# Kernel tuning notes

Hardware: AMD Instinct MI355X
Metric: run time of the kernel (lower is better)

The kernel has to match this reference:

```python
import jax, jax.numpy as jnp
import numpy as np

EPS = 1e-6

def _rms_norm(x, w):
    rms = jnp.sqrt(jnp.mean(x * x, axis=-1, keepdims=True) + EPS)
    return x / rms * w

def _rotate_half(x):
    x1, x2 = jnp.split(x, 2, axis=-1)
    return jnp.concatenate([-x2, x1], axis=-1)

def _apply_rope(qk, cos, sin):
    return qk * cos + _rotate_half(qk) * sin

def setup_inputs() -> dict:
    key = jax.random.key(0)
    ks = jax.random.split(key, 4)
    B, N, C, H = 4, 2048, 1024, 16
    hd = C // H
    x = jax.random.normal(ks[0], (B, N, C), dtype=jnp.float32)
    rope_cos = jax.random.uniform(ks[1], (1, 1, N, hd), dtype=jnp.float32)
    rope_sin = jax.random.uniform(ks[2], (1, 1, N, hd), dtype=jnp.float32)
    w_qkv = jax.random.normal(ks[3], (3 * C, C), dtype=jnp.float32) * (C ** -0.5)
    w_proj = jax.random.normal(jax.random.fold_in(key, 10), (C, C), dtype=jnp.float32) * (C ** -0.5)
    b_proj = jnp.zeros((C,), dtype=jnp.float32)
    q_norm_w = jnp.ones((hd,), dtype=jnp.float32)
    k_norm_w = jnp.ones((hd,), dtype=jnp.float32)
    return {"x": x, "rope_cos": rope_cos, "rope_sin": rope_sin, "w_qkv": w_qkv,
            "w_proj": w_proj, "b_proj": b_proj, "q_norm_w": q_norm_w, "k_norm_w": k_norm_w}

def reference(x, rope_cos, rope_sin, w_qkv, w_proj, b_proj, q_norm_w, k_norm_w):
    B, N, C = x.shape
    H = 16
    hd = C // H
    scale = hd ** -0.5
    qkv = jnp.einsum('bnc,dc->bnd', x, w_qkv)          # [B,N,3C]
    qkv = qkv.reshape(B, N, 3, H, hd).transpose(2, 0, 3, 1, 4)  # [3,B,H,N,hd]
    q, k, v = qkv[0], qkv[1], qkv[2]
    q = _rms_norm(q, q_norm_w)
    k = _rms_norm(k, k_norm_w)
    q = _apply_rope(q, rope_cos, rope_sin)
    k = _apply_rope(k, rope_cos, rope_sin)
    attn = jnp.einsum('bhqd,bhkd->bhqk', q, k) * scale
    attn = jax.nn.softmax(attn, axis=-1)
    out = jnp.einsum('bhqk,bhkd->bhqd', attn, v)        # [B,H,N,hd]
    out = out.transpose(0, 2, 1, 3).reshape(B, N, C)
    return jnp.einsum('bnc,dc->bnd', out, w_proj) + b_proj
```

## Files before the change

kernel.cpp:

```cpp
#include <hip/hip_runtime.h>
#include <stdint.h>
#include <math.h>

typedef unsigned short u16;
typedef __attribute__((ext_vector_type(8))) short short8;
typedef __attribute__((ext_vector_type(4))) float floatx4;
typedef __attribute__((ext_vector_type(4))) unsigned short ushort4v;

#define MFMA16(a, b, c) __builtin_amdgcn_mfma_f32_16x16x32_bf16(a, b, c, 0, 0, 0)

constexpr int B_ = 4, N_ = 2048, C_ = 1024, H_ = 16, HD = 64;
constexpr size_t SZ_X = (size_t)B_ * N_ * C_;
constexpr size_t SZ_WQKV = (size_t)3 * C_ * C_;
constexpr size_t SZ_WPROJ = (size_t)C_ * C_;
constexpr size_t SZ_QKV = (size_t)B_ * H_ * N_ * HD;

#define QSCALE 0.1803368801111204f

__device__ __forceinline__ u16 f2bf(float f) {
  union { float f; uint32_t u; } c; c.f = f;
  uint32_t u = c.u;
  return (u16)((u + 0x7FFFu + ((u >> 16) & 1u)) >> 16);
}
__device__ __forceinline__ uint32_t p2b(float s) {
  return (uint32_t)(int)__builtin_fmaf(s, 128.0f, 16250.91f);
}
__device__ __forceinline__ void async16(const u16* g, u16* l) {
  __builtin_amdgcn_global_load_lds(
      (const __attribute__((address_space(1))) void*)g,
      (__attribute__((address_space(3))) void*)l, 16, 0, 0);
}

__global__ __launch_bounds__(256) void cvt_bf16(const float* __restrict__ in,
                                                u16* __restrict__ out, int n4) {
  int i = blockIdx.x * 256 + threadIdx.x;
  if (i >= n4) return;
  float4 v = ((const float4*)in)[i];
  ushort4v o;
  o.x = f2bf(v.x); o.y = f2bf(v.y); o.z = f2bf(v.z); o.w = f2bf(v.w);
  ((ushort4v*)out)[i] = o;
}

template <int MODE>
__global__ __launch_bounds__(256) void gemm_bt(
    const u16* __restrict__ A, const u16* __restrict__ Bm, int K,
    u16* __restrict__ qb, u16* __restrict__ kb, u16* __restrict__ vtb,
    float* __restrict__ outf, const float* __restrict__ bias, int N,
    const float* __restrict__ cosp, const float* __restrict__ sinp,
    const float* __restrict__ qw, const float* __restrict__ kw) {
  const int tid = threadIdx.x;
  const int wave = tid >> 6;
  const int lane = tid & 63;
  const int quad = lane >> 4;
  const int l16 = lane & 15;
  const int id = blockIdx.x + blockIdx.y * 64;
  const int bm0 = ((id & 7) * 8 + ((id >> 3) & 7)) * 128;
  const int bn0 = (id >> 6) * 128;
  const int wm = (wave >> 1) * 64;
  const int wn = (wave & 1) * 64;

  __shared__ __align__(16) u16 As[2][128 * 32];
  __shared__ __align__(16) u16 Bs[2][128 * 32];

  floatx4 acc[4][4];
#pragma unroll
  for (int i = 0; i < 4; ++i)
#pragma unroll
    for (int j = 0; j < 4; ++j)
#pragma unroll
      for (int r = 0; r < 4; ++r) acc[i][j][r] = 0.f;

  auto stage = [&](int k0, int buf) {
#pragma unroll
    for (int j = 0; j < 2; ++j) {
      const int seg = tid + j * 256;
      const int row = seg >> 2;
      const int ks = (seg & 3) * 8;
      u16* la = As[buf] + (size_t)(wave * 64 + j * 256) * 8;
      u16* lb = Bs[buf] + (size_t)(wave * 64 + j * 256) * 8;
      async16(A + (size_t)(bm0 + row) * K + k0 + ks, la);
      async16(Bm + (size_t)(bn0 + row) * K + k0 + ks, lb);
    }
  };

  const int niter = K >> 5;
  stage(0, 0);
  for (int kt = 0; kt < niter; ++kt) {
    __syncthreads();
    if (kt + 1 < niter) stage((kt + 1) << 5, (kt + 1) & 1);
    const u16* as = As[kt & 1];
    const u16* bs = Bs[kt & 1];

    short8 af[4], bf[4];
#pragma unroll
    for (int t = 0; t < 4; ++t)
      af[t] = *(const short8*)(as + (wm + t * 16 + l16) * 32 + quad * 8);
#pragma unroll
    for (int t = 0; t < 4; ++t)
      bf[t] = *(const short8*)(bs + (wn + t * 16 + l16) * 32 + quad * 8);
#pragma unroll
    for (int i = 0; i < 4; ++i)
#pragma unroll
      for (int j = 0; j < 4; ++j)
        acc[i][j] = MFMA16(af[i], bf[j], acc[i][j]);
  }

  if (MODE == 0) {
    const int hb = (bn0 + wn) >> 6;
    const int t = hb >> 4;
    const int h = hb & 15;
    if (t < 2) {
      const float* w = (t == 0) ? qw : kw;
      u16* dstb = (t == 0) ? qb : kb;
      float wv[4];
#pragma unroll
      for (int j = 0; j < 4; ++j) wv[j] = w[j * 16 + l16];
#pragma unroll
      for (int i = 0; i < 4; ++i)
#pragma unroll
        for (int r = 0; r < 4; ++r) {
          const int m = bm0 + wm + i * 16 + quad * 4 + r;
          const int b = m >> 11, tok = m & 2047;
          float ss = 0.f;
#pragma unroll
          for (int j = 0; j < 4; ++j) ss += acc[i][j][r] * acc[i][j][r];
          ss += __shfl_xor(ss, 1);
          ss += __shfl_xor(ss, 2);
          ss += __shfl_xor(ss, 4);
          ss += __shfl_xor(ss, 8);
          const float inv = 1.0f / sqrtf(ss * (1.0f / 64.0f) + 1e-6f);
          float xn[4];
#pragma unroll
          for (int j = 0; j < 4; ++j) xn[j] = acc[i][j][r] * inv * wv[j];
          u16* dst = dstb + ((size_t)(b * 16 + h) * 2048 + tok) * 64;
#pragma unroll
          for (int j = 0; j < 4; ++j) {
            const int e = j * 16 + l16;
            const float cs = cosp[tok * 64 + e];
            const float sn = sinp[tok * 64 + e];
            const float rot = (j < 2) ? -xn[j + 2] : xn[j - 2];
            float o = xn[j] * cs + rot * sn;
            if (t == 0) o *= QSCALE;
            dst[e] = f2bf(o);
          }
        }
    } else {
#pragma unroll
      for (int i = 0; i < 4; ++i)
#pragma unroll
        for (int j = 0; j < 4; ++j)
#pragma unroll
          for (int r = 0; r < 4; ++r) {
            const int m = bm0 + wm + i * 16 + quad * 4 + r;
            const int b = m >> 11, tok = m & 2047;
            const int e = j * 16 + l16;
            vtb[((size_t)(b * 16 + h) * 64 + e) * 2048 + tok] =
                f2bf(acc[i][j][r]);
          }
    }
  } else {
#pragma unroll
    for (int i = 0; i < 4; ++i)
#pragma unroll
      for (int j = 0; j < 4; ++j)
#pragma unroll
        for (int r = 0; r < 4; ++r) {
          const int m = bm0 + wm + i * 16 + quad * 4 + r;
          const int n = bn0 + wn + j * 16 + l16;
          outf[(size_t)m * N + n] = acc[i][j][r] + bias[n];
        }
  }
}

__global__ __launch_bounds__(256) void attn_kernel(
    const u16* __restrict__ qb, const u16* __restrict__ kb,
    const u16* __restrict__ vtb, u16* __restrict__ ob) {
  const int tid = threadIdx.x;
  const int wave = tid >> 6, lane = tid & 63;
  const int quad = lane >> 4, l16 = lane & 15;

  const int id = blockIdx.x + blockIdx.y * 16;
  const int bh = (id & 7) + 8 * ((id >> 3) & 7);
  const int q0 = (id >> 6) * 128;

  __shared__ __align__(16) u16 Ksf[2][64 * 64];
  __shared__ __align__(16) u16 Vsf[2][64 * 64];
  __shared__ __align__(16) u16 Ps[4][2][16 * 72];

  const u16* qptr = qb + (size_t)bh * (2048 * 64);
  const u16* kptr = kb + (size_t)bh * (2048 * 64);
  const u16* vptr = vtb + (size_t)bh * (64 * 2048);

  const int s0 = tid, s1 = tid + 256;
  const int ct0 = s0 >> 7, ct1 = s1 >> 7;
  const int hf0 = (s0 >> 6) & 1, hf1 = (s1 >> 6) & 1;
  const u16* kg0 = kptr + (size_t)(ct0 * 16 + l16) * 64 + hf0 * 32 + quad * 8;
  const u16* kg1 = kptr + (size_t)(ct1 * 16 + l16) * 64 + hf1 * 32 + quad * 8;
  const u16* vg0 = vptr + (size_t)(ct0 * 16 + l16) * 2048 + hf0 * 32 + quad * 8;
  const u16* vg1 = vptr + (size_t)(ct1 * 16 + l16) * 2048 + hf1 * 32 + quad * 8;
  const int lo0 = (wave * 64) * 8;
  const int lo1 = (256 + wave * 64) * 8;

  short8 aq[2][2];
#pragma unroll
  for (int sub = 0; sub < 2; ++sub) {
    const int qrow = q0 + wave * 32 + sub * 16 + l16;
#pragma unroll
    for (int hf = 0; hf < 2; ++hf)
      aq[sub][hf] =
          *(const short8*)(qptr + (size_t)qrow * 64 + hf * 32 + quad * 8);
  }

  short8 ones;
#pragma unroll
  for (int j = 0; j < 8; ++j) ones[j] = (short)0x3F80;

  floatx4 o[2][4], ol[2];
#pragma unroll
  for (int sub = 0; sub < 2; ++sub) {
#pragma unroll
    for (int r = 0; r < 4; ++r) ol[sub][r] = 0.f;
#pragma unroll
    for (int et = 0; et < 4; ++et)
#pragma unroll
      for (int r = 0; r < 4; ++r) o[sub][et][r] = 0.f;
  }

  async16(kg0, Ksf[0] + lo0);
  async16(kg1, Ksf[0] + lo1);
  async16(vg0, Vsf[0] + lo0);
  async16(vg1, Vsf[0] + lo1);

  for (int it = 0; it < 32; ++it) {
    __syncthreads();
    if (it + 1 < 32) {
      const int n1 = (it + 1) * 64;
      const int b1 = (it + 1) & 1;
      async16(kg0 + (size_t)n1 * 64, Ksf[b1] + lo0);
      async16(kg1 + (size_t)n1 * 64, Ksf[b1] + lo1);
      async16(vg0 + n1, Vsf[b1] + lo0);
      async16(vg1 + n1, Vsf[b1] + lo1);
    }
    const u16* Kt = Ksf[it & 1];
    const u16* Vt = Vsf[it & 1];

#pragma unroll
    for (int t = 0; t < 4; ++t) {
      const short8 kf0 = *(const short8*)(Kt + t * 1024 + lane * 8);
      const short8 kf1 = *(const short8*)(Kt + t * 1024 + 512 + lane * 8);
#pragma unroll
      for (int sub = 0; sub < 2; ++sub) {
        floatx4 z;
#pragma unroll
        for (int r = 0; r < 4; ++r) z[r] = 0.f;
        z = MFMA16(kf0, aq[sub][0], z);
        z = MFMA16(kf1, aq[sub][1], z);
        uint2 w;
        w.x = p2b(z[0]) | (p2b(z[1]) << 16);
        w.y = p2b(z[2]) | (p2b(z[3]) << 16);
        *(uint2*)(Ps[wave][sub] + l16 * 72 + t * 16 + quad * 4) = w;
      }
    }

    __asm__ volatile("s_waitcnt lgkmcnt(0)" ::: "memory");

    short8 pa[2][2];
#pragma unroll
    for (int sub = 0; sub < 2; ++sub) {
      pa[sub][0] = *(const short8*)(Ps[wave][sub] + l16 * 72 + quad * 8);
      pa[sub][1] = *(const short8*)(Ps[wave][sub] + l16 * 72 + 32 + quad * 8);
    }

#pragma unroll
    for (int et = 0; et < 4; ++et) {
      const short8 vb0 = *(const short8*)(Vt + et * 1024 + lane * 8);
      const short8 vb1 = *(const short8*)(Vt + et * 1024 + 512 + lane * 8);
#pragma unroll
      for (int sub = 0; sub < 2; ++sub) {
        o[sub][et] = MFMA16(pa[sub][0], vb0, o[sub][et]);
        o[sub][et] = MFMA16(pa[sub][1], vb1, o[sub][et]);
      }
    }
#pragma unroll
    for (int sub = 0; sub < 2; ++sub) {
      ol[sub] = MFMA16(pa[sub][0], ones, ol[sub]);
      ol[sub] = MFMA16(pa[sub][1], ones, ol[sub]);
    }
  }

  const int b = bh >> 4, h = bh & 15;
#pragma unroll
  for (int sub = 0; sub < 2; ++sub) {
    float inv[4];
#pragma unroll
    for (int r = 0; r < 4; ++r) inv[r] = 1.0f / ol[sub][r];
#pragma unroll
    for (int et = 0; et < 4; ++et)
#pragma unroll
      for (int r = 0; r < 4; ++r) {
        const int row = q0 + wave * 32 + sub * 16 + quad * 4 + r;
        const int e = et * 16 + l16;
        ob[((size_t)b * 2048 + row) * 1024 + h * 64 + e] =
            f2bf(o[sub][et][r] * inv[r]);
      }
  }
}

extern "C" void kernel_launch(void* const* d_in, const int* in_sizes, int n_in,
                              void* d_out, int out_size, void* d_ws, size_t ws_size,
                              hipStream_t stream) {
  const float* x     = (const float*)d_in[0];
  const float* cosp  = (const float*)d_in[1];
  const float* sinp  = (const float*)d_in[2];
  const float* wqkv  = (const float*)d_in[3];
  const float* wproj = (const float*)d_in[4];
  const float* bias  = (const float*)d_in[5];
  const float* qw    = (const float*)d_in[6];
  const float* kw    = (const float*)d_in[7];
  float* out = (float*)d_out;

  u16* xb     = (u16*)d_ws;
  u16* wqkvb  = xb + SZ_X;
  u16* wprojb = wqkvb + SZ_WQKV;
  u16* qb     = wprojb + SZ_WPROJ;
  u16* kb     = qb + SZ_QKV;
  u16* vtb    = kb + SZ_QKV;
  u16* ob     = vtb + SZ_QKV;

  cvt_bf16<<<(int)(SZ_X / 4 / 256), 256, 0, stream>>>(x, xb, (int)(SZ_X / 4));
  cvt_bf16<<<(int)(SZ_WQKV / 4 / 256), 256, 0, stream>>>(wqkv, wqkvb, (int)(SZ_WQKV / 4));
  cvt_bf16<<<(int)(SZ_WPROJ / 4 / 256), 256, 0, stream>>>(wproj, wprojb, (int)(SZ_WPROJ / 4));

  gemm_bt<0><<<dim3(64, 24), 256, 0, stream>>>(xb, wqkvb, 1024, qb, kb, vtb,
                                               nullptr, nullptr, 3072,
                                               cosp, sinp, qw, kw);
  attn_kernel<<<dim3(16, 64), 256, 0, stream>>>(qb, kb, vtb, ob);
  gemm_bt<1><<<dim3(64, 8), 256, 0, stream>>>(ob, wprojb, 1024, nullptr, nullptr,
                                              nullptr, out, bias, 1024,
                                              nullptr, nullptr, nullptr, nullptr);
}
```

Baseline: 305.0 us.

## Pre-swizzle K/V into MFMA fragment layout and load V directly from global

The QKV GEMM epilogue now writes K and V^T in a tile-blocked layout that matches the MFMA fragment order, so the attention kernel copies K contiguously into LDS and reads V fragments straight from global memory into registers without staging through shared memory. This removes the V LDS buffer and halves the async copies per iteration, and launch bounds now request 4 blocks per CU for higher occupancy. The three conversion kernels are also merged into one launch to cut launch overhead. In exchange, the epilogue stores become more scattered, and V global loads sit on the critical path without LDS double-buffering, relying on occupancy to hide their latency.

```diff
diff --git a/kernel.cpp b/kernel.cpp
--- a/kernel.cpp
+++ b/kernel.cpp
@@ -31,14 +31,22 @@
       (__attribute__((address_space(3))) void*)l, 16, 0, 0);
 }
 
-__global__ __launch_bounds__(256) void cvt_bf16(const float* __restrict__ in,
-                                                u16* __restrict__ out, int n4) {
+__global__ __launch_bounds__(256) void cvt_all(
+    const float* __restrict__ x, const float* __restrict__ wqkv,
+    const float* __restrict__ wproj, u16* __restrict__ xb,
+    u16* __restrict__ wqkvb, u16* __restrict__ wprojb) {
+  const int n1 = (int)(SZ_X / 4), n2 = (int)(SZ_WQKV / 4);
   int i = blockIdx.x * 256 + threadIdx.x;
-  if (i >= n4) return;
-  float4 v = ((const float4*)in)[i];
+  const float* src;
+  u16* dst;
+  int k;
+  if (i < n1) { src = x; dst = xb; k = i; }
+  else if (i < n1 + n2) { src = wqkv; dst = wqkvb; k = i - n1; }
+  else { src = wproj; dst = wprojb; k = i - n1 - n2; }
+  float4 v = ((const float4*)src)[k];
   ushort4v o;
   o.x = f2bf(v.x); o.y = f2bf(v.y); o.z = f2bf(v.z); o.w = f2bf(v.w);
-  ((ushort4v*)out)[i] = o;
+  ((ushort4v*)dst)[k] = o;
 }
 
 template <int MODE>
@@ -111,7 +119,6 @@
     const int h = hb & 15;
     if (t < 2) {
       const float* w = (t == 0) ? qw : kw;
-      u16* dstb = (t == 0) ? qb : kb;
       float wv[4];
 #pragma unroll
       for (int j = 0; j < 4; ++j) wv[j] = w[j * 16 + l16];
@@ -132,7 +139,7 @@
           float xn[4];
 #pragma unroll
           for (int j = 0; j < 4; ++j) xn[j] = acc[i][j][r] * inv * wv[j];
-          u16* dst = dstb + ((size_t)(b * 16 + h) * 2048 + tok) * 64;
+          const size_t bh = (size_t)(b * 16 + h);
 #pragma unroll
           for (int j = 0; j < 4; ++j) {
             const int e = j * 16 + l16;
@@ -140,8 +147,15 @@
             const float sn = sinp[tok * 64 + e];
             const float rot = (j < 2) ? -xn[j + 2] : xn[j - 2];
             float o = xn[j] * cs + rot * sn;
-            if (t == 0) o *= QSCALE;
-            dst[e] = f2bf(o);
+            if (t == 0) {
+              qb[(bh * 2048 + tok) * 64 + e] = f2bf(o * QSCALE);
+            } else {
+              const int kt2 = tok >> 6, t3 = (tok >> 4) & 3;
+              const int hf = j >> 1;
+              const int qf = (j & 1) * 2 + (l16 >> 3);
+              kb[bh * 131072 + (size_t)kt2 * 4096 + (t3 * 2 + hf) * 512 +
+                 (qf * 16 + (tok & 15)) * 8 + (l16 & 7)] = f2bf(o);
+            }
           }
         }
     } else {
@@ -153,8 +167,10 @@
           for (int r = 0; r < 4; ++r) {
             const int m = bm0 + wm + i * 16 + quad * 4 + r;
             const int b = m >> 11, tok = m & 2047;
-            const int e = j * 16 + l16;
-            vtb[((size_t)(b * 16 + h) * 64 + e) * 2048 + tok] =
+            const int kt2 = tok >> 6, nn = tok & 63;
+            const int hf = nn >> 5, qf = (nn & 31) >> 3, jf = nn & 7;
+            vtb[(size_t)(b * 16 + h) * 131072 + (size_t)kt2 * 4096 +
+                (j * 2 + hf) * 512 + (qf * 16 + l16) * 8 + jf] =
                 f2bf(acc[i][j][r]);
           }
     }
@@ -172,7 +188,7 @@
   }
 }
 
-__global__ __launch_bounds__(256) void attn_kernel(
+__global__ __launch_bounds__(256, 4) void attn_kernel(
     const u16* __restrict__ qb, const u16* __restrict__ kb,
     const u16* __restrict__ vtb, u16* __restrict__ ob) {
   const int tid = threadIdx.x;
@@ -184,20 +200,13 @@
   const int q0 = (id >> 6) * 128;
 
   __shared__ __align__(16) u16 Ksf[2][64 * 64];
-  __shared__ __align__(16) u16 Vsf[2][64 * 64];
   __shared__ __align__(16) u16 Ps[4][2][16 * 72];
 
   const u16* qptr = qb + (size_t)bh * (2048 * 64);
-  const u16* kptr = kb + (size_t)bh * (2048 * 64);
-  const u16* vptr = vtb + (size_t)bh * (64 * 2048);
+  const u16* kptr = kb + (size_t)bh * 131072;
+  const u16* vptr = vtb + (size_t)bh * 131072;
 
   const int s0 = tid, s1 = tid + 256;
-  const int ct0 = s0 >> 7, ct1 = s1 >> 7;
-  const int hf0 = (s0 >> 6) & 1, hf1 = (s1 >> 6) & 1;
-  const u16* kg0 = kptr + (size_t)(ct0 * 16 + l16) * 64 + hf0 * 32 + quad * 8;
-  const u16* kg1 = kptr + (size_t)(ct1 * 16 + l16) * 64 + hf1 * 32 + quad * 8;
-  const u16* vg0 = vptr + (size_t)(ct0 * 16 + l16) * 2048 + hf0 * 32 + quad * 8;
-  const u16* vg1 = vptr + (size_t)(ct1 * 16 + l16) * 2048 + hf1 * 32 + quad * 8;
   const int lo0 = (wave * 64) * 8;
   const int lo1 = (256 + wave * 64) * 8;
 
@@ -226,23 +235,27 @@
       for (int r = 0; r < 4; ++r) o[sub][et][r] = 0.f;
   }
 
-  async16(kg0, Ksf[0] + lo0);
-  async16(kg1, Ksf[0] + lo1);
-  async16(vg0, Vsf[0] + lo0);
-  async16(vg1, Vsf[0] + lo1);
+  async16(kptr + (size_t)s0 * 8, Ksf[0] + lo0);
+  async16(kptr + (size_t)s1 * 8, Ksf[0] + lo1);
 
   for (int it = 0; it < 32; ++it) {
     __syncthreads();
     if (it + 1 < 32) {
-      const int n1 = (it + 1) * 64;
+      const u16* kt = kptr + (size_t)(it + 1) * 4096;
       const int b1 = (it + 1) & 1;
-      async16(kg0 + (size_t)n1 * 64, Ksf[b1] + lo0);
-      async16(kg1 + (size_t)n1 * 64, Ksf[b1] + lo1);
-      async16(vg0 + n1, Vsf[b1] + lo0);
-      async16(vg1 + n1, Vsf[b1] + lo1);
+      async16(kt + (size_t)s0 * 8, Ksf[b1] + lo0);
+      async16(kt + (size_t)s1 * 8, Ksf[b1] + lo1);
     }
     const u16* Kt = Ksf[it & 1];
-    const u16* Vt = Vsf[it & 1];
+
+    const u16* vt = vptr + (size_t)it * 4096;
+    short8 vf[4][2];
+#pragma unroll
+    for (int et = 0; et < 4; ++et)
+#pragma unroll
+      for (int hf = 0; hf < 2; ++hf)
+        vf[et][hf] =
+            *(const short8*)(vt + (et * 2 + hf) * 512 + lane * 8);
 
 #pragma unroll
     for (int t = 0; t < 4; ++t) {
@@ -272,15 +285,12 @@
     }
 
 #pragma unroll
-    for (int et = 0; et < 4; ++et) {
-      const short8 vb0 = *(const short8*)(Vt + et * 1024 + lane * 8);
-      const short8 vb1 = *(const short8*)(Vt + et * 1024 + 512 + lane * 8);
+    for (int et = 0; et < 4; ++et)
 #pragma unroll
       for (int sub = 0; sub < 2; ++sub) {
-        o[sub][et] = MFMA16(pa[sub][0], vb0, o[sub][et]);
-        o[sub][et] = MFMA16(pa[sub][1], vb1, o[sub][et]);
+        o[sub][et] = MFMA16(pa[sub][0], vf[et][0], o[sub][et]);
+        o[sub][et] = MFMA16(pa[sub][1], vf[et][1], o[sub][et]);
       }
-    }
 #pragma unroll
     for (int sub = 0; sub < 2; ++sub) {
       ol[sub] = MFMA16(pa[sub][0], ones, ol[sub]);
@@ -327,9 +337,8 @@
   u16* vtb    = kb + SZ_QKV;
   u16* ob     = vtb + SZ_QKV;
 
-  cvt_bf16<<<(int)(SZ_X / 4 / 256), 256, 0, stream>>>(x, xb, (int)(SZ_X / 4));
-  cvt_bf16<<<(int)(SZ_WQKV / 4 / 256), 256, 0, stream>>>(wqkv, wqkvb, (int)(SZ_WQKV / 4));
-  cvt_bf16<<<(int)(SZ_WPROJ / 4 / 256), 256, 0, stream>>>(wproj, wprojb, (int)(SZ_WPROJ / 4));
+  const int ncvt = (int)((SZ_X + SZ_WQKV + SZ_WPROJ) / 4 / 256);
+  cvt_all<<<ncvt, 256, 0, stream>>>(x, wqkv, wproj, xb, wqkvb, wprojb);
 
   gemm_bt<0><<<dim3(64, 24), 256, 0, stream>>>(xb, wqkvb, 1024, qb, kb, vtb,
                                                nullptr, nullptr, 3072,
```

Result: faster. 296.8 us (-2.7%).
